# Kernel optimization log

Measured on AMD Instinct MI355X. Metric: run time of the kernel, lower is better.

Reference implementation:

```python
import jax, jax.numpy as jnp
import numpy as np

B, T, C, HEAD_SIZE = 512, 128, 1024, 128
BLOCK_SIZE = 128  # module's registered tril buffer size


def setup_inputs() -> dict:
    key = jax.random.key(0)
    k0, k1, k2, k3 = jax.random.split(key, 4)
    idx = jax.random.normal(k0, (B, T, C), dtype=jnp.float32)
    # torch Linear(note_dimensions, head_size, bias=False); stored here as [in, out]
    Wk = jax.random.normal(k1, (C, HEAD_SIZE), dtype=jnp.float32) * 0.02
    Wq = jax.random.normal(k2, (C, HEAD_SIZE), dtype=jnp.float32) * 0.02
    Wv = jax.random.normal(k3, (C, HEAD_SIZE), dtype=jnp.float32) * 0.02
    return {"idx": idx, "Wk": Wk, "Wq": Wq, "Wv": Wv}


def reference(idx, Wk, Wq, Wv):
    # q, k, v: [B, T, H]
    k = idx @ Wk
    q = idx @ Wq
    v = idx @ Wv
    # NOTE: original multiplies by head_size**0.5 (not divides) - kept faithful.
    weights = jnp.einsum('bth,bsh->bts', q, k) * (HEAD_SIZE ** 0.5)  # [B, T, T]
    causal = jnp.tril(jnp.ones((T, T), dtype=bool))
    weights = jnp.where(causal, weights, -jnp.inf)
    # NOTE: original applies softmax over dim=1 (query axis) - kept faithful.
    activations = jax.nn.softmax(weights, axis=1)
    # dropout is identity in eval/reference mode
    out = jnp.einsum('bts,bsh->bth', activations, v)  # [B, T, H]
    return out
```

## Files before the change

### kernel.cpp

```cpp
#include <hip/hip_runtime.h>
#include <hip/hip_bf16.h>


typedef __attribute__((ext_vector_type(8))) __bf16 bf16x8;
typedef __attribute__((ext_vector_type(4))) float f32x4;
typedef __attribute__((ext_vector_type(4))) unsigned short u16x4;
typedef __attribute__((ext_vector_type(8))) unsigned short u16x8;

#define SQRT_H 11.313708498984761f

__device__ __forceinline__ void splitf(float a, unsigned short& hi, unsigned short& lo) {
    unsigned u = __float_as_uint(a);
    hi = (unsigned short)(u >> 16);
    float r = a - __uint_as_float(u & 0xFFFF0000u);
    lo = (unsigned short)(__float_as_uint(r) >> 16);
}

__global__ __launch_bounds__(256) void prep_w(
    const float* __restrict__ Wq, const float* __restrict__ Wk, const float* __restrict__ Wv,
    unsigned short* __restrict__ W2hi, unsigned short* __restrict__ W2lo)
{
    __shared__ __align__(16) unsigned short thi[128][128];
    __shared__ __align__(16) unsigned short tlo[128][128];
    const float* W = (blockIdx.y == 0) ? Wq : (blockIdx.y == 1 ? Wk : Wv);
    const int c0 = blockIdx.x * 128;
    const int tid = threadIdx.x;
    #pragma unroll
    for (int it = 0; it < 16; ++it) {
        int chunk = tid + it * 256;
        int cl = chunk >> 5, f4 = chunk & 31;
        float4 v = *(const float4*)(W + (size_t)(c0 + cl) * 128 + f4 * 4);
        unsigned short h, l;
        splitf(v.x, h, l); thi[cl][f4*4+0] = h; tlo[cl][f4*4+0] = l;
        splitf(v.y, h, l); thi[cl][f4*4+1] = h; tlo[cl][f4*4+1] = l;
        splitf(v.z, h, l); thi[cl][f4*4+2] = h; tlo[cl][f4*4+2] = l;
        splitf(v.w, h, l); thi[cl][f4*4+3] = h; tlo[cl][f4*4+3] = l;
    }
    __syncthreads();
    #pragma unroll
    for (int it = 0; it < 8; ++it) {
        int chunk = tid + it * 256;
        int h = chunk >> 4, slot = chunk & 15;
        u16x8 vh, vl;
        #pragma unroll
        for (int e = 0; e < 8; ++e) { vh[e] = thi[slot*8+e][h]; vl[e] = tlo[slot*8+e][h]; }
        size_t off = (size_t)(blockIdx.y * 128 + h) * 1024 + c0 + slot * 8;
        *(u16x8*)(W2hi + off) = vh;
        *(u16x8*)(W2lo + off) = vl;
    }
}

__global__ __launch_bounds__(256, 2) void qkv_gemm(
    const float* __restrict__ idx,
    const unsigned short* __restrict__ W2hi, const unsigned short* __restrict__ W2lo,
    float* __restrict__ qo, float* __restrict__ ko, float* __restrict__ vT)
{
    __shared__ __align__(16) char smem[65536];
    const int tid  = threadIdx.x;
    const int lane = tid & 63;
    const int wid  = tid >> 6;
    const int wr = wid >> 1, wc = wid & 1;
    const int l16 = lane & 15, lgr = lane >> 4;
    const int bx = blockIdx.x;
    const int mt = bx / 3;
    const int nt = bx - mt * 3;

    f32x4 acc[4][4];
    #pragma unroll
    for (int m = 0; m < 4; ++m)
        #pragma unroll
        for (int n = 0; n < 4; ++n) acc[m][n] = (f32x4){0.f, 0.f, 0.f, 0.f};

    const float* Ag = idx + (size_t)mt * (128 * 1024);
    const unsigned short* Bhg = W2hi + (size_t)nt * 128 * 1024;
    const unsigned short* Blg = W2lo + (size_t)nt * 128 * 1024;

    for (int ks = 0; ks < 1024; ks += 64) {
        __syncthreads();
        #pragma unroll
        for (int it = 0; it < 8; ++it) {
            int chunk = tid + it * 256;
            int row = chunk >> 4, f4 = chunk & 15;
            float4 v = *(const float4*)(Ag + (size_t)row * 1024 + ks + f4 * 4);
            unsigned short h0,h1,h2,h3,l0,l1,l2,l3;
            splitf(v.x,h0,l0); splitf(v.y,h1,l1); splitf(v.z,h2,l2); splitf(v.w,h3,l3);
            u16x4 hv = {h0,h1,h2,h3}, lv = {l0,l1,l2,l3};
            int off = row * 128 + ((f4 * 8) ^ ((row & 7) << 4));
            *(u16x4*)(smem + off)         = hv;
            *(u16x4*)(smem + 16384 + off) = lv;
        }
        #pragma unroll
        for (int it = 0; it < 4; ++it) {
            int chunk = tid + it * 256;
            int row = chunk >> 3, slot = chunk & 7;
            size_t goff = (size_t)row * 1024 + ks + slot * 8;
            u16x8 bh = *(const u16x8*)(Bhg + goff);
            u16x8 bl = *(const u16x8*)(Blg + goff);
            int off = row * 128 + ((slot * 16) ^ ((row & 7) << 4));
            *(u16x8*)(smem + 32768 + off) = bh;
            *(u16x8*)(smem + 49152 + off) = bl;
        }
        __syncthreads();
        #pragma unroll
        for (int kk = 0; kk < 64; kk += 32) {
            const int kbyte = (kk + lgr * 8) * 2;
            bf16x8 ahi[4], alo[4], bhi[4], blo[4];
            #pragma unroll
            for (int m = 0; m < 4; ++m) {
                int row = wr * 64 + m * 16 + l16;
                int off = row * 128 + (kbyte ^ ((row & 7) << 4));
                ahi[m] = *(const bf16x8*)(smem + off);
                alo[m] = *(const bf16x8*)(smem + 16384 + off);
            }
            #pragma unroll
            for (int n = 0; n < 4; ++n) {
                int row = wc * 64 + n * 16 + l16;
                int off = row * 128 + (kbyte ^ ((row & 7) << 4));
                bhi[n] = *(const bf16x8*)(smem + 32768 + off);
                blo[n] = *(const bf16x8*)(smem + 49152 + off);
            }
            #pragma unroll
            for (int m = 0; m < 4; ++m)
                #pragma unroll
                for (int n = 0; n < 4; ++n) {
                    acc[m][n] = __builtin_amdgcn_mfma_f32_16x16x32_bf16(ahi[m], bhi[n], acc[m][n], 0, 0, 0);
                    acc[m][n] = __builtin_amdgcn_mfma_f32_16x16x32_bf16(alo[m], bhi[n], acc[m][n], 0, 0, 0);
                    acc[m][n] = __builtin_amdgcn_mfma_f32_16x16x32_bf16(ahi[m], blo[n], acc[m][n], 0, 0, 0);
                }
        }
    }
    if (nt == 2) {
        float* outp = vT + (size_t)mt * (128 * 128);
        #pragma unroll
        for (int m = 0; m < 4; ++m)
            #pragma unroll
            for (int n = 0; n < 4; ++n) {
                int t = wr * 64 + m * 16 + lgr * 4;
                int h = wc * 64 + n * 16 + l16;
                *(f32x4*)(outp + (size_t)h * 128 + t) = acc[m][n];
            }
    } else {
        float* outp = (nt == 0 ? qo : ko) + (size_t)mt * (128 * 128);
        #pragma unroll
        for (int m = 0; m < 4; ++m)
            #pragma unroll
            for (int n = 0; n < 4; ++n)
                #pragma unroll
                for (int j = 0; j < 4; ++j) {
                    int t = wr * 64 + m * 16 + lgr * 4 + j;
                    int h = wc * 64 + n * 16 + l16;
                    outp[(size_t)t * 128 + h] = acc[m][n][j];
                }
    }
}

__global__ __launch_bounds__(512, 2) void attn(
    const float* __restrict__ qg, const float* __restrict__ kg,
    const float* __restrict__ vTg, float* __restrict__ outg)
{
    __shared__ __align__(16) char smem[135680];
    float* S    = (float*)(smem);
    float* scrM = (float*)(smem + 131072);
    float* scrS = (float*)(smem + 133120);
    float* scrD = (float*)(smem + 135168);

    const int tid  = threadIdx.x;
    const int lane = tid & 63;
    const int wid  = tid >> 6;
    const int wr = wid >> 2, wc = wid & 3;
    const int l16 = lane & 15, lgr = lane >> 4;
    const int b = blockIdx.x;

    const float* qb = qg  + (size_t)b * 16384;
    const float* kb = kg  + (size_t)b * 16384;
    const float* vb = vTg + (size_t)b * 16384;

    #pragma unroll
    for (int it = 0; it < 8; ++it) {
        int chunk = tid + it * 512;
        int row = chunk >> 5, f4 = chunk & 31;
        float4 vq = *(const float4*)(qb + (size_t)row * 128 + f4 * 4);
        float4 vk = *(const float4*)(kb + (size_t)row * 128 + f4 * 4);
        unsigned short h0,h1,h2,h3,l0,l1,l2,l3;
        int off = row * 256 + ((f4 * 8) ^ ((row & 7) << 4));
        splitf(vq.x,h0,l0); splitf(vq.y,h1,l1); splitf(vq.z,h2,l2); splitf(vq.w,h3,l3);
        *(u16x4*)(smem + off)         = (u16x4){h0,h1,h2,h3};
        *(u16x4*)(smem + 32768 + off) = (u16x4){l0,l1,l2,l3};
        splitf(vk.x,h0,l0); splitf(vk.y,h1,l1); splitf(vk.z,h2,l2); splitf(vk.w,h3,l3);
        *(u16x4*)(smem + 65536 + off) = (u16x4){h0,h1,h2,h3};
        *(u16x4*)(smem + 98304 + off) = (u16x4){l0,l1,l2,l3};
    }
    __syncthreads();

    f32x4 accs[4][2];
    #pragma unroll
    for (int m = 0; m < 4; ++m) { accs[m][0] = (f32x4){0.f,0.f,0.f,0.f}; accs[m][1] = (f32x4){0.f,0.f,0.f,0.f}; }
    #pragma unroll
    for (int kk = 0; kk < 128; kk += 32) {
        const int kbyte = (kk + lgr * 8) * 2;
        bf16x8 qh[4], ql[4], kh[2], kl[2];
        #pragma unroll
        for (int m = 0; m < 4; ++m) {
            int row = wr * 64 + m * 16 + l16;
            int off = row * 256 + (kbyte ^ ((row & 7) << 4));
            qh[m] = *(const bf16x8*)(smem + off);
            ql[m] = *(const bf16x8*)(smem + 32768 + off);
        }
        #pragma unroll
        for (int n = 0; n < 2; ++n) {
            int row = wc * 32 + n * 16 + l16;
            int off = row * 256 + (kbyte ^ ((row & 7) << 4));
            kh[n] = *(const bf16x8*)(smem + 65536 + off);
            kl[n] = *(const bf16x8*)(smem + 98304 + off);
        }
        #pragma unroll
        for (int m = 0; m < 4; ++m)
            #pragma unroll
            for (int n = 0; n < 2; ++n) {
                accs[m][n] = __builtin_amdgcn_mfma_f32_16x16x32_bf16(qh[m], kh[n], accs[m][n], 0, 0, 0);
                accs[m][n] = __builtin_amdgcn_mfma_f32_16x16x32_bf16(ql[m], kh[n], accs[m][n], 0, 0, 0);
                accs[m][n] = __builtin_amdgcn_mfma_f32_16x16x32_bf16(qh[m], kl[n], accs[m][n], 0, 0, 0);
            }
    }
    __syncthreads();

    #pragma unroll
    for (int m = 0; m < 4; ++m)
        #pragma unroll
        for (int n = 0; n < 2; ++n)
            #pragma unroll
            for (int j = 0; j < 4; ++j) {
                int t = wr * 64 + m * 16 + lgr * 4 + j;
                int s = wc * 32 + n * 16 + l16;
                float val = accs[m][n][j] * SQRT_H;
                S[t * 128 + s] = (t >= s) ? val : -1e30f;
            }
    __syncthreads();

    const int scol = tid & 127;
    const int qtr  = tid >> 7;
    const int t0   = qtr * 32;
    float mloc = -1e30f;
    for (int t = t0; t < t0 + 32; ++t) mloc = fmaxf(mloc, S[t * 128 + scol]);
    scrM[tid] = mloc;
    __syncthreads();
    float mm = fmaxf(fmaxf(scrM[scol], scrM[128 + scol]), fmaxf(scrM[256 + scol], scrM[384 + scol]));
    float sum = 0.f;
    for (int t = t0; t < t0 + 32; ++t) {
        float e = __expf(S[t * 128 + scol] - mm);
        sum += e;
        unsigned short hi, lo; splitf(e, hi, lo);
        int off = t * 256 + ((scol * 2) ^ ((t & 7) << 4));
        *(unsigned short*)(smem + 65536 + off) = hi;
        *(unsigned short*)(smem + 98304 + off) = lo;
    }
    scrS[tid] = sum;
    __syncthreads();
    if (tid < 128) {
        float d = scrS[tid] + scrS[128 + tid] + scrS[256 + tid] + scrS[384 + tid];
        scrD[tid] = 1.f / d;
    }
    __syncthreads();

    #pragma unroll
    for (int it = 0; it < 8; ++it) {
        int chunk = tid + it * 512;
        int row = chunk >> 5, f4 = chunk & 31;
        float4 vv = *(const float4*)(vb + (size_t)row * 128 + f4 * 4);
        vv.x *= scrD[f4 * 4 + 0]; vv.y *= scrD[f4 * 4 + 1];
        vv.z *= scrD[f4 * 4 + 2]; vv.w *= scrD[f4 * 4 + 3];
        unsigned short h0,h1,h2,h3,l0,l1,l2,l3;
        splitf(vv.x,h0,l0); splitf(vv.y,h1,l1); splitf(vv.z,h2,l2); splitf(vv.w,h3,l3);
        int off = row * 256 + ((f4 * 8) ^ ((row & 7) << 4));
        *(u16x4*)(smem + off)         = (u16x4){h0,h1,h2,h3};
        *(u16x4*)(smem + 32768 + off) = (u16x4){l0,l1,l2,l3};
    }
    __syncthreads();

    f32x4 acco[4][2];
    #pragma unroll
    for (int m = 0; m < 4; ++m) { acco[m][0] = (f32x4){0.f,0.f,0.f,0.f}; acco[m][1] = (f32x4){0.f,0.f,0.f,0.f}; }
    #pragma unroll
    for (int kk = 0; kk < 128; kk += 32) {
        const int kbyte = (kk + lgr * 8) * 2;
        bf16x8 ah[4], al[4], vh[2], vl[2];
        #pragma unroll
        for (int m = 0; m < 4; ++m) {
            int row = wr * 64 + m * 16 + l16;
            int off = row * 256 + (kbyte ^ ((row & 7) << 4));
            ah[m] = *(const bf16x8*)(smem + 65536 + off);
            al[m] = *(const bf16x8*)(smem + 98304 + off);
        }
        #pragma unroll
        for (int n = 0; n < 2; ++n) {
            int row = wc * 32 + n * 16 + l16;
            int off = row * 256 + (kbyte ^ ((row & 7) << 4));
            vh[n] = *(const bf16x8*)(smem + off);
            vl[n] = *(const bf16x8*)(smem + 32768 + off);
        }
        #pragma unroll
        for (int m = 0; m < 4; ++m)
            #pragma unroll
            for (int n = 0; n < 2; ++n) {
                acco[m][n] = __builtin_amdgcn_mfma_f32_16x16x32_bf16(ah[m], vh[n], acco[m][n], 0, 0, 0);
                acco[m][n] = __builtin_amdgcn_mfma_f32_16x16x32_bf16(al[m], vh[n], acco[m][n], 0, 0, 0);
                acco[m][n] = __builtin_amdgcn_mfma_f32_16x16x32_bf16(ah[m], vl[n], acco[m][n], 0, 0, 0);
            }
    }
    float* ob = outg + (size_t)b * 16384;
    #pragma unroll
    for (int m = 0; m < 4; ++m)
        #pragma unroll
        for (int n = 0; n < 2; ++n)
            #pragma unroll
            for (int j = 0; j < 4; ++j) {
                int t = wr * 64 + m * 16 + lgr * 4 + j;
                int h = wc * 32 + n * 16 + l16;
                ob[(size_t)t * 128 + h] = acco[m][n][j];
            }
}

extern "C" void kernel_launch(void* const* d_in, const int* in_sizes, int n_in,
                              void* d_out, int out_size, void* d_ws, size_t ws_size,
                              hipStream_t stream) {
    const float* idx = (const float*)d_in[0];
    const float* Wk  = (const float*)d_in[1];
    const float* Wq  = (const float*)d_in[2];
    const float* Wv  = (const float*)d_in[3];
    float* out = (float*)d_out;

    char* ws = (char*)d_ws;
    float* qb = (float*)(ws);
    float* kb = (float*)(ws + 33554432);
    float* vT = (float*)(ws + 67108864);
    unsigned short* W2hi = (unsigned short*)(ws + 100663296);
    unsigned short* W2lo = (unsigned short*)(ws + 101449728);

    prep_w<<<dim3(8, 3), 256, 0, stream>>>(Wq, Wk, Wv, W2hi, W2lo);
    qkv_gemm<<<dim3(512 * 3), 256, 0, stream>>>(idx, W2hi, W2lo, qb, kb, vT);
    attn<<<dim3(512), 512, 0, stream>>>(qb, kb, vT, out);
}
```

Measured before the change: 501.1 us.

## Keep softmax in registers, stream Q/V fragments from global, remap GEMM blocks

The attention kernel no longer stages the full fp32 score matrix in shared memory. The column softmax (over the query axis) is now computed in registers using wave shuffles and a small cross-wave scratch. Q and V fragments are loaded straight from global memory and split into bf16 hi/lo inside the MFMA loops, with 1/sum applied to the probabilities rather than to V. This cuts LDS from about 135KB to about 67KB so the launch bound can request 4 blocks per CU, at the cost of redundant global loads and splits. The QKV GEMM also remaps block IDs so that the blocks sharing a row tile are spread across XCDs.

New measurement: 499.7 us. No clear change (-0.3%).

```diff
diff --git a/kernel.cpp b/kernel.cpp
--- a/kernel.cpp
+++ b/kernel.cpp
@@ -61,9 +61,10 @@
     const int wid  = tid >> 6;
     const int wr = wid >> 1, wc = wid & 1;
     const int l16 = lane & 15, lgr = lane >> 4;
-    const int bx = blockIdx.x;
-    const int mt = bx / 3;
-    const int nt = bx - mt * 3;
+    const int hw = blockIdx.x;
+    const int logical = (hw & 7) * 192 + (hw >> 3);
+    const int mt = logical / 3;
+    const int nt = logical - mt * 3;
 
     f32x4 acc[4][4];
     #pragma unroll
@@ -154,15 +155,13 @@
     }
 }
 
-__global__ __launch_bounds__(512, 2) void attn(
+__global__ __launch_bounds__(512, 4) void attn(
     const float* __restrict__ qg, const float* __restrict__ kg,
     const float* __restrict__ vTg, float* __restrict__ outg)
 {
-    __shared__ __align__(16) char smem[135680];
-    float* S    = (float*)(smem);
-    float* scrM = (float*)(smem + 131072);
-    float* scrS = (float*)(smem + 133120);
-    float* scrD = (float*)(smem + 135168);
+    __shared__ __align__(16) char smem[67584];
+    float* scrM = (float*)(smem + 65536);
+    float* scrS = (float*)(smem + 66560);
 
     const int tid  = threadIdx.x;
     const int lane = tid & 63;
@@ -179,16 +178,12 @@
     for (int it = 0; it < 8; ++it) {
         int chunk = tid + it * 512;
         int row = chunk >> 5, f4 = chunk & 31;
-        float4 vq = *(const float4*)(qb + (size_t)row * 128 + f4 * 4);
         float4 vk = *(const float4*)(kb + (size_t)row * 128 + f4 * 4);
         unsigned short h0,h1,h2,h3,l0,l1,l2,l3;
+        splitf(vk.x,h0,l0); splitf(vk.y,h1,l1); splitf(vk.z,h2,l2); splitf(vk.w,h3,l3);
         int off = row * 256 + ((f4 * 8) ^ ((row & 7) << 4));
-        splitf(vq.x,h0,l0); splitf(vq.y,h1,l1); splitf(vq.z,h2,l2); splitf(vq.w,h3,l3);
         *(u16x4*)(smem + off)         = (u16x4){h0,h1,h2,h3};
         *(u16x4*)(smem + 32768 + off) = (u16x4){l0,l1,l2,l3};
-        splitf(vk.x,h0,l0); splitf(vk.y,h1,l1); splitf(vk.z,h2,l2); splitf(vk.w,h3,l3);
-        *(u16x4*)(smem + 65536 + off) = (u16x4){h0,h1,h2,h3};
-        *(u16x4*)(smem + 98304 + off) = (u16x4){l0,l1,l2,l3};
     }
     __syncthreads();
 
@@ -198,32 +193,38 @@
     #pragma unroll
     for (int kk = 0; kk < 128; kk += 32) {
         const int kbyte = (kk + lgr * 8) * 2;
-        bf16x8 qh[4], ql[4], kh[2], kl[2];
-        #pragma unroll
-        for (int m = 0; m < 4; ++m) {
-            int row = wr * 64 + m * 16 + l16;
-            int off = row * 256 + (kbyte ^ ((row & 7) << 4));
-            qh[m] = *(const bf16x8*)(smem + off);
-            ql[m] = *(const bf16x8*)(smem + 32768 + off);
-        }
+        bf16x8 kh[2], kl[2];
         #pragma unroll
         for (int n = 0; n < 2; ++n) {
             int row = wc * 32 + n * 16 + l16;
             int off = row * 256 + (kbyte ^ ((row & 7) << 4));
-            kh[n] = *(const bf16x8*)(smem + 65536 + off);
-            kl[n] = *(const bf16x8*)(smem + 98304 + off);
-        }
-        #pragma unroll
-        for (int m = 0; m < 4; ++m)
+            kh[n] = *(const bf16x8*)(smem + off);
+            kl[n] = *(const bf16x8*)(smem + 32768 + off);
+        }
+        #pragma unroll
+        for (int m = 0; m < 4; ++m) {
+            int trow = wr * 64 + m * 16 + l16;
+            float4 a0 = *(const float4*)(qb + trow * 128 + kk + lgr * 8);
+            float4 a1 = *(const float4*)(qb + trow * 128 + kk + lgr * 8 + 4);
+            unsigned short hh[8], ll[8];
+            splitf(a0.x,hh[0],ll[0]); splitf(a0.y,hh[1],ll[1]);
+            splitf(a0.z,hh[2],ll[2]); splitf(a0.w,hh[3],ll[3]);
+            splitf(a1.x,hh[4],ll[4]); splitf(a1.y,hh[5],ll[5]);
+            splitf(a1.z,hh[6],ll[6]); splitf(a1.w,hh[7],ll[7]);
+            u16x8 qh8 = {hh[0],hh[1],hh[2],hh[3],hh[4],hh[5],hh[6],hh[7]};
+            u16x8 ql8 = {ll[0],ll[1],ll[2],ll[3],ll[4],ll[5],ll[6],ll[7]};
+            bf16x8 qh = *(bf16x8*)&qh8, ql = *(bf16x8*)&ql8;
             #pragma unroll
             for (int n = 0; n < 2; ++n) {
-                accs[m][n] = __builtin_amdgcn_mfma_f32_16x16x32_bf16(qh[m], kh[n], accs[m][n], 0, 0, 0);
-                accs[m][n] = __builtin_amdgcn_mfma_f32_16x16x32_bf16(ql[m], kh[n], accs[m][n], 0, 0, 0);
-                accs[m][n] = __builtin_amdgcn_mfma_f32_16x16x32_bf16(qh[m], kl[n], accs[m][n], 0, 0, 0);
-            }
-    }
-    __syncthreads();
-
+                accs[m][n] = __builtin_amdgcn_mfma_f32_16x16x32_bf16(qh, kh[n], accs[m][n], 0, 0, 0);
+                accs[m][n] = __builtin_amdgcn_mfma_f32_16x16x32_bf16(ql, kh[n], accs[m][n], 0, 0, 0);
+                accs[m][n] = __builtin_amdgcn_mfma_f32_16x16x32_bf16(qh, kl[n], accs[m][n], 0, 0, 0);
+            }
+        }
+    }
+    __syncthreads();
+
+    float cmax[2] = {-3e38f, -3e38f};
     #pragma unroll
     for (int m = 0; m < 4; ++m)
         #pragma unroll
@@ -233,48 +234,65 @@
                 int t = wr * 64 + m * 16 + lgr * 4 + j;
                 int s = wc * 32 + n * 16 + l16;
                 float val = accs[m][n][j] * SQRT_H;
-                S[t * 128 + s] = (t >= s) ? val : -1e30f;
-            }
-    __syncthreads();
-
-    const int scol = tid & 127;
-    const int qtr  = tid >> 7;
-    const int t0   = qtr * 32;
-    float mloc = -1e30f;
-    for (int t = t0; t < t0 + 32; ++t) mloc = fmaxf(mloc, S[t * 128 + scol]);
-    scrM[tid] = mloc;
-    __syncthreads();
-    float mm = fmaxf(fmaxf(scrM[scol], scrM[128 + scol]), fmaxf(scrM[256 + scol], scrM[384 + scol]));
-    float sum = 0.f;
-    for (int t = t0; t < t0 + 32; ++t) {
-        float e = __expf(S[t * 128 + scol] - mm);
-        sum += e;
-        unsigned short hi, lo; splitf(e, hi, lo);
-        int off = t * 256 + ((scol * 2) ^ ((t & 7) << 4));
-        *(unsigned short*)(smem + 65536 + off) = hi;
-        *(unsigned short*)(smem + 98304 + off) = lo;
-    }
-    scrS[tid] = sum;
-    __syncthreads();
-    if (tid < 128) {
-        float d = scrS[tid] + scrS[128 + tid] + scrS[256 + tid] + scrS[384 + tid];
-        scrD[tid] = 1.f / d;
-    }
-    __syncthreads();
-
-    #pragma unroll
-    for (int it = 0; it < 8; ++it) {
-        int chunk = tid + it * 512;
-        int row = chunk >> 5, f4 = chunk & 31;
-        float4 vv = *(const float4*)(vb + (size_t)row * 128 + f4 * 4);
-        vv.x *= scrD[f4 * 4 + 0]; vv.y *= scrD[f4 * 4 + 1];
-        vv.z *= scrD[f4 * 4 + 2]; vv.w *= scrD[f4 * 4 + 3];
-        unsigned short h0,h1,h2,h3,l0,l1,l2,l3;
-        splitf(vv.x,h0,l0); splitf(vv.y,h1,l1); splitf(vv.z,h2,l2); splitf(vv.w,h3,l3);
-        int off = row * 256 + ((f4 * 8) ^ ((row & 7) << 4));
-        *(u16x4*)(smem + off)         = (u16x4){h0,h1,h2,h3};
-        *(u16x4*)(smem + 32768 + off) = (u16x4){l0,l1,l2,l3};
-    }
+                val = (t >= s) ? val : -1e30f;
+                accs[m][n][j] = val;
+                cmax[n] = fmaxf(cmax[n], val);
+            }
+    #pragma unroll
+    for (int n = 0; n < 2; ++n) {
+        cmax[n] = fmaxf(cmax[n], __shfl_xor(cmax[n], 16));
+        cmax[n] = fmaxf(cmax[n], __shfl_xor(cmax[n], 32));
+    }
+    if (lgr == 0) {
+        scrM[(wr * 4 + wc) * 32 + l16]      = cmax[0];
+        scrM[(wr * 4 + wc) * 32 + 16 + l16] = cmax[1];
+    }
+    __syncthreads();
+    float mm[2];
+    #pragma unroll
+    for (int n = 0; n < 2; ++n)
+        mm[n] = fmaxf(scrM[wc * 32 + n * 16 + l16], scrM[(4 + wc) * 32 + n * 16 + l16]);
+
+    float csum[2] = {0.f, 0.f};
+    #pragma unroll
+    for (int m = 0; m < 4; ++m)
+        #pragma unroll
+        for (int n = 0; n < 2; ++n)
+            #pragma unroll
+            for (int j = 0; j < 4; ++j) {
+                float e = __expf(accs[m][n][j] - mm[n]);
+                accs[m][n][j] = e;
+                csum[n] += e;
+            }
+    #pragma unroll
+    for (int n = 0; n < 2; ++n) {
+        csum[n] += __shfl_xor(csum[n], 16);
+        csum[n] += __shfl_xor(csum[n], 32);
+    }
+    if (lgr == 0) {
+        scrS[(wr * 4 + wc) * 32 + l16]      = csum[0];
+        scrS[(wr * 4 + wc) * 32 + 16 + l16] = csum[1];
+    }
+    __syncthreads();
+    float inv[2];
+    #pragma unroll
+    for (int n = 0; n < 2; ++n)
+        inv[n] = 1.f / (scrS[wc * 32 + n * 16 + l16] + scrS[(4 + wc) * 32 + n * 16 + l16]);
+
+    #pragma unroll
+    for (int m = 0; m < 4; ++m)
+        #pragma unroll
+        for (int n = 0; n < 2; ++n)
+            #pragma unroll
+            for (int j = 0; j < 4; ++j) {
+                int t = wr * 64 + m * 16 + lgr * 4 + j;
+                int s = wc * 32 + n * 16 + l16;
+                float a = accs[m][n][j] * inv[n];
+                unsigned short hi, lo; splitf(a, hi, lo);
+                int off = t * 256 + ((s * 2) ^ ((t & 7) << 4));
+                *(unsigned short*)(smem + off)         = hi;
+                *(unsigned short*)(smem + 32768 + off) = lo;
+            }
     __syncthreads();
 
     f32x4 acco[4][2];
@@ -283,29 +301,34 @@
     #pragma unroll
     for (int kk = 0; kk < 128; kk += 32) {
         const int kbyte = (kk + lgr * 8) * 2;
-        bf16x8 ah[4], al[4], vh[2], vl[2];
+        bf16x8 vh[2], vl[2];
+        #pragma unroll
+        for (int n = 0; n < 2; ++n) {
+            int hrow = wc * 32 + n * 16 + l16;
+            float4 v0 = *(const float4*)(vb + hrow * 128 + kk + lgr * 8);
+            float4 v1 = *(const float4*)(vb + hrow * 128 + kk + lgr * 8 + 4);
+            unsigned short hh[8], ll[8];
+            splitf(v0.x,hh[0],ll[0]); splitf(v0.y,hh[1],ll[1]);
+            splitf(v0.z,hh[2],ll[2]); splitf(v0.w,hh[3],ll[3]);
+            splitf(v1.x,hh[4],ll[4]); splitf(v1.y,hh[5],ll[5]);
+            splitf(v1.z,hh[6],ll[6]); splitf(v1.w,hh[7],ll[7]);
+            u16x8 vh8 = {hh[0],hh[1],hh[2],hh[3],hh[4],hh[5],hh[6],hh[7]};
+            u16x8 vl8 = {ll[0],ll[1],ll[2],ll[3],ll[4],ll[5],ll[6],ll[7]};
+            vh[n] = *(bf16x8*)&vh8; vl[n] = *(bf16x8*)&vl8;
+        }
         #pragma unroll
         for (int m = 0; m < 4; ++m) {
-            int row = wr * 64 + m * 16 + l16;
-            int off = row * 256 + (kbyte ^ ((row & 7) << 4));
-            ah[m] = *(const bf16x8*)(smem + 65536 + off);
-            al[m] = *(const bf16x8*)(smem + 98304 + off);
-        }
-        #pragma unroll
-        for (int n = 0; n < 2; ++n) {
-            int row = wc * 32 + n * 16 + l16;
-            int off = row * 256 + (kbyte ^ ((row & 7) << 4));
-            vh[n] = *(const bf16x8*)(smem + off);
-            vl[n] = *(const bf16x8*)(smem + 32768 + off);
-        }
-        #pragma unroll
-        for (int m = 0; m < 4; ++m)
+            int arow = wr * 64 + m * 16 + l16;
+            int off = arow * 256 + (kbyte ^ ((arow & 7) << 4));
+            bf16x8 ah = *(const bf16x8*)(smem + off);
+            bf16x8 al = *(const bf16x8*)(smem + 32768 + off);
             #pragma unroll
             for (int n = 0; n < 2; ++n) {
-                acco[m][n] = __builtin_amdgcn_mfma_f32_16x16x32_bf16(ah[m], vh[n], acco[m][n], 0, 0, 0);
-                acco[m][n] = __builtin_amdgcn_mfma_f32_16x16x32_bf16(al[m], vh[n], acco[m][n], 0, 0, 0);
-                acco[m][n] = __builtin_amdgcn_mfma_f32_16x16x32_bf16(ah[m], vl[n], acco[m][n], 0, 0, 0);
-            }
+                acco[m][n] = __builtin_amdgcn_mfma_f32_16x16x32_bf16(ah, vh[n], acco[m][n], 0, 0, 0);
+                acco[m][n] = __builtin_amdgcn_mfma_f32_16x16x32_bf16(al, vh[n], acco[m][n], 0, 0, 0);
+                acco[m][n] = __builtin_amdgcn_mfma_f32_16x16x32_bf16(ah, vl[n], acco[m][n], 0, 0, 0);
+            }
+        }
     }
     float* ob = outg + (size_t)b * 16384;
     #pragma unroll
```
